# Kernel tuning notes

Measured on AMD Instinct MI355X. Metric: run time of the kernel, lower is better.

## Reference

```python
import jax, jax.numpy as jnp
import numpy as np

H = 768; R = 16; L = 3; NS = 128; NQ = 128


def setup_inputs():
    key = jax.random.key(0)
    ks = iter(jax.random.split(key, 40))
    def w(shape, s=0.02):
        return (s * jax.random.normal(next(ks), shape)).astype(jnp.float32)
    return {
        "support_features": jax.random.normal(next(ks), (NS, H), jnp.float32),
        "support_labels": jax.random.randint(next(ks), (NS,), 0, 3),
        "query_features": jax.random.normal(next(ks), (NQ, H), jnp.float32),
        "sim_w1": w((H, 2 * H)), "sim_b1": jnp.zeros((H,), jnp.float32),
        "sim_w2": w((R, H)), "sim_b2": jnp.zeros((R,), jnp.float32),
        "div_w1": w((H, 2 * H)), "div_b1": jnp.zeros((H,), jnp.float32),
        "div_w2": w((R, H)), "div_b2": jnp.zeros((R,), jnp.float32),
        "rel_w": w((L, R, H, H)), "rel_b": jnp.zeros((L, R, H), jnp.float32),
        "agg_w1": w((L, H, 2 * H)), "agg_b1": jnp.zeros((L, H), jnp.float32),
        "agg_w2": w((L, H, H)), "agg_b2": jnp.zeros((L, H), jnp.float32),
        "ln_g": jnp.ones((L, H), jnp.float32), "ln_b": jnp.zeros((L, H), jnp.float32),
        "cls_w1": w((H // 2, H)), "cls_b1": jnp.zeros((H // 2,), jnp.float32),
        "cls_w2": w((3, H // 2)), "cls_b2": jnp.zeros((3,), jnp.float32),
    }


def _symmetrize(F):
    # torch loop fills [i,j] and [j,i] with value computed from pair (min(i,j), max(i,j)); diag stays 0
    N = F.shape[0]
    idx = jnp.arange(N)
    lower = (idx[:, None] > idx[None, :])
    Fs = jnp.where(lower[:, :, None], jnp.swapaxes(F, 0, 1), F)
    off = (idx[:, None] != idx[None, :]).astype(F.dtype)
    return Fs * off[:, :, None]


def _relations(x, w1, b1, w2, b2, diversity):
    h = x.shape[1]
    wa, wb = w1[:, :h], w1[:, h:]  # split concat([a,b]) @ w1^T into two matmuls
    pa = x @ wa.T                  # [N,H], contribution of first element (x_i)
    if diversity:
        d = jnp.abs(x[:, None, :] - x[None, :, :])   # [N,N,H]
        hid = jax.nn.relu(pa[:, None, :] + d @ wb.T + b1)
    else:
        pb = x @ wb.T
        hid = jax.nn.relu(pa[:, None, :] + pb[None, :, :] + b1)
    logits = hid @ w2.T + b2       # [N,N,R]
    return _symmetrize(jax.nn.softmax(logits, axis=-1))


def _layer_norm(y, g, b):
    mu = y.mean(-1, keepdims=True)
    var = ((y - mu) ** 2).mean(-1, keepdims=True)
    return (y - mu) / jnp.sqrt(var + 1e-5) * g + b


def _prop_layer(x, C, rw, rb, aw1, ab1, aw2, ab2, g, b):
    N = x.shape[0]
    T = jnp.einsum('jh,rkh->jrk', x, rw) + rb       # per-relation transform [N,R,H]
    msg = jnp.einsum('ijr,jrk->ik', C, T) / (N - 1)  # mean over N-1 neighbors (diag of C is 0)
    comb = jnp.concatenate([x, msg], axis=-1)
    agg = jax.nn.relu(comb @ aw1.T + ab1) @ aw2.T + ab2
    return _layer_norm(agg + x, g, b)


def reference(support_features, support_labels, query_features,
              sim_w1, sim_b1, sim_w2, sim_b2,
              div_w1, div_b1, div_w2, div_b2,
              rel_w, rel_b, agg_w1, agg_b1, agg_w2, agg_b2, ln_g, ln_b,
              cls_w1, cls_b1, cls_w2, cls_b2):
    all_x = jnp.concatenate([support_features, query_features], axis=0)
    sim = _relations(all_x, sim_w1, sim_b1, sim_w2, sim_b2, diversity=False)
    div = _relations(all_x, div_w1, div_b1, div_w2, div_b2, diversity=True)
    C = (sim + div) * 0.5
    x = all_x
    for l in range(L):
        x = _prop_layer(x, C, rel_w[l], rel_b[l], agg_w1[l], agg_b1[l],
                        agg_w2[l], agg_b2[l], ln_g[l], ln_b[l])
    q = x[support_features.shape[0]:]
    preds = jax.nn.relu(q @ cls_w1.T + cls_b1) @ cls_w2.T + cls_b2  # dropout = identity (eval)
    return preds, sim, div, x
```

## Files before the change

kernel.cpp:

```cpp
#include <hip/hip_runtime.h>
#include <hip/hip_bf16.h>


typedef __attribute__((ext_vector_type(8))) short s16x8;
typedef __attribute__((ext_vector_type(4))) float f32x4;

__device__ __forceinline__ short f2bf_s(float f){
  union { __hip_bfloat16 h; short s; } u; u.h = __float2bfloat16(f); return u.s;
}
__device__ __forceinline__ float bf_s2f(short s){
  union { __hip_bfloat16 h; short s; } u; u.s = s; return __bfloat162float(u.h);
}
__device__ __forceinline__ f32x4 mfma16(s16x8 a, s16x8 b, f32x4 c){
  return __builtin_amdgcn_mfma_f32_16x16x32_bf16(a, b, c, 0, 0, 0);
}
__device__ __forceinline__ void gload16(void* lds, const void* g){
  __builtin_amdgcn_global_load_lds((const __attribute__((address_space(1))) void*)g,
                                   (__attribute__((address_space(3))) void*)lds,
                                   16, 0, 0);
}
__device__ __forceinline__ unsigned pack2bf(float lo, float hi){
  return __builtin_amdgcn_perm(__float_as_uint(hi), __float_as_uint(lo), 0x07060302u);
}
__device__ __forceinline__ s16x8 absdiff_bf(uint4 a, uint4 b){
  union { s16x8 v; unsigned u[4]; } o;
  const unsigned au[4] = {a.x,a.y,a.z,a.w}, bu[4] = {b.x,b.y,b.z,b.w};
  #pragma unroll
  for (int w = 0; w < 4; ++w){
    float dlo = __uint_as_float(au[w] << 16)         - __uint_as_float(bu[w] << 16);
    float dhi = __uint_as_float(au[w] & 0xffff0000u) - __uint_as_float(bu[w] & 0xffff0000u);
    unsigned r;
    asm("v_cvt_pk_bf16_f32 %0, abs(%1), abs(%2)" : "=v"(r) : "v"(dlo), "v"(dhi));
    o.u[w] = r;
  }
  return o.v;
}

__device__ __forceinline__ void tri_decode(int b, int& i0, int& j0){
  int jb = (int)((sqrtf(2.f*(float)b + 1.f) - 1.f)*0.5f);
  while (2*(jb+1)*(jb+2) <= b) ++jb;
  while (2*jb*(jb+1) > b) --jb;
  i0 = (b - 2*jb*(jb+1))*4;
  j0 = jb*16;
}

template<int BM, int BN, int EPI>
__global__ __launch_bounds__(256) void gemm_bt2(
    const short* __restrict__ A, int lda,
    const short* __restrict__ B, int ldb,
    float* __restrict__ Cf, short* __restrict__ Cb, int ldc,
    const float* __restrict__ bias, int K, int NT)
{
  __shared__ short As[BM*128];
  __shared__ short Bs[BN*128];
  const int tid = threadIdx.x, lane = tid & 63, wid = tid >> 6;
  const int nt = blockIdx.x % NT, mt = blockIdx.x / NT;
  const int m0 = mt*BM, n0 = nt*BN;
  const int wm0 = (wid>>1)*(BM/2), wn0 = (wid&1)*(BN/2);
  f32x4 acc[BM/32][BN/32] = {};
  for (int k0 = 0; k0 < K; k0 += 128){
    if (k0) __syncthreads();
    #pragma unroll
    for (int q = 0; q < BM/16; ++q){
      const int d = (wid*(BM/16)+q)*1024 + lane*16;
      const int row = d>>8, c = d&255;
      gload16((char*)As + (wid*(BM/16)+q)*1024,
              (const char*)A + (size_t)(m0+row)*lda*2 + (size_t)k0*2 + (c ^ ((row&7)<<4)));
    }
    #pragma unroll
    for (int q = 0; q < BN/16; ++q){
      const int d = (wid*(BN/16)+q)*1024 + lane*16;
      const int row = d>>8, c = d&255;
      gload16((char*)Bs + (wid*(BN/16)+q)*1024,
              (const char*)B + (size_t)(n0+row)*ldb*2 + (size_t)k0*2 + (c ^ ((row&7)<<4)));
    }
    __syncthreads();
    #pragma unroll
    for (int kk = 0; kk < 4; ++kk){
      const int colb = (kk*32 + (lane>>4)*8)*2;
      s16x8 af[BM/32], bfv[BN/32];
      #pragma unroll
      for (int mi = 0; mi < BM/32; ++mi){
        const int row = wm0 + mi*16 + (lane&15);
        af[mi] = *(const s16x8*)((char*)As + row*256 + (colb ^ ((row&7)<<4)));
      }
      #pragma unroll
      for (int ni = 0; ni < BN/32; ++ni){
        const int row = wn0 + ni*16 + (lane&15);
        bfv[ni] = *(const s16x8*)((char*)Bs + row*256 + (colb ^ ((row&7)<<4)));
      }
      #pragma unroll
      for (int mi = 0; mi < BM/32; ++mi)
        #pragma unroll
        for (int ni = 0; ni < BN/32; ++ni)
          acc[mi][ni] = mfma16(af[mi], bfv[ni], acc[mi][ni]);
    }
  }
  #pragma unroll
  for (int mi = 0; mi < BM/32; ++mi){
    #pragma unroll
    for (int ni = 0; ni < BN/32; ++ni){
      const int gcol = n0 + wn0 + ni*16 + (lane&15);
      const float bv = bias[gcol];
      #pragma unroll
      for (int r = 0; r < 4; ++r){
        const int grow = m0 + wm0 + mi*16 + (lane>>4)*4 + r;
        float v = acc[mi][ni][r] + bv;
        if (EPI == 2) v = fmaxf(v, 0.f);
        if (EPI == 3) Cf[(size_t)grow*ldc + gcol] = v;
        else          Cb[(size_t)grow*ldc + gcol] = f2bf_s(v);
      }
    }
  }
}

__global__ __launch_bounds__(256) void gemm_msg(
    const short* __restrict__ A,
    const short* __restrict__ B,
    float* __restrict__ slabs)
{
  __shared__ short As[64*64];
  __shared__ short Bs[64*64];
  const int tid = threadIdx.x, lane = tid & 63, wid = tid >> 6;
  const int mt = blockIdx.x / 12, nt = blockIdx.x % 12;
  const int m0 = mt*64, n0 = nt*64, kc0 = blockIdx.y*512;
  const int wm0 = (wid>>1)*32, wn0 = (wid&1)*32;
  f32x4 acc[2][2] = {};
  for (int s = 0; s < 8; ++s){
    const int k0 = kc0 + s*64;
    if (s) __syncthreads();
    #pragma unroll
    for (int q = 0; q < 2; ++q){
      const int d = (wid*2+q)*1024 + lane*16;
      const int row = d>>7, c = d&127;
      gload16((char*)As + (wid*2+q)*1024,
              (const char*)A + (size_t)(m0+row)*8192 + (size_t)k0*2 + (c ^ ((row&7)<<4)));
    }
    #pragma unroll
    for (int rd = 0; rd < 2; ++rd){
      int ei = rd*2048 + tid*8, kr = ei>>6, nc = ei&63;
      union { uint4 v; short s4[8]; } u;
      u.v = *(const uint4*)(B + (size_t)(k0+kr)*768 + n0 + nc);
      #pragma unroll
      for (int e = 0; e < 8; ++e)
        *(short*)((char*)Bs + (nc+e)*128 + ((kr*2) ^ (((nc+e)&7)<<4))) = u.s4[e];
    }
    __syncthreads();
    #pragma unroll
    for (int kk = 0; kk < 2; ++kk){
      const int colb = (kk*32 + (lane>>4)*8)*2;
      s16x8 af[2], bfv[2];
      #pragma unroll
      for (int mi = 0; mi < 2; ++mi){
        const int row = wm0 + mi*16 + (lane&15);
        af[mi] = *(const s16x8*)((char*)As + row*128 + (colb ^ ((row&7)<<4)));
      }
      #pragma unroll
      for (int ni = 0; ni < 2; ++ni){
        const int row = wn0 + ni*16 + (lane&15);
        bfv[ni] = *(const s16x8*)((char*)Bs + row*128 + (colb ^ ((row&7)<<4)));
      }
      #pragma unroll
      for (int mi = 0; mi < 2; ++mi)
        #pragma unroll
        for (int ni = 0; ni < 2; ++ni)
          acc[mi][ni] = mfma16(af[mi], bfv[ni], acc[mi][ni]);
    }
  }
  float* out = slabs + (size_t)blockIdx.y*196608;
  #pragma unroll
  for (int mi = 0; mi < 2; ++mi)
    #pragma unroll
    for (int ni = 0; ni < 2; ++ni){
      const int gcol = n0 + wn0 + ni*16 + (lane&15);
      #pragma unroll
      for (int r = 0; r < 4; ++r){
        const int grow = m0 + wm0 + mi*16 + (lane>>4)*4 + r;
        out[(size_t)grow*768 + gcol] = acc[mi][ni][r];
      }
    }
}

__global__ void msgsum(const float* __restrict__ slabs, short* __restrict__ comb){
  const int i = (blockIdx.x*256 + threadIdx.x)*4;
  if (i >= 196608) return;
  float4 s = {0.f,0.f,0.f,0.f};
  #pragma unroll
  for (int c = 0; c < 8; ++c){
    float4 v = *(const float4*)(slabs + (size_t)c*196608 + i);
    s.x += v.x; s.y += v.y; s.z += v.z; s.w += v.w;
  }
  const float sc = 1.f/255.f;
  const int row = i/768, col = i%768;
  union { uint2 u; short s4[4]; } o;
  o.s4[0]=f2bf_s(s.x*sc); o.s4[1]=f2bf_s(s.y*sc);
  o.s4[2]=f2bf_s(s.z*sc); o.s4[3]=f2bf_s(s.w*sc);
  *(uint2*)(comb + (size_t)row*1536 + 768 + col) = o.u;
}

__device__ __forceinline__ void stageB(short* dstbase, const short* Bsrc,
                                       int n0, int k0, int wv, int lane){
  #pragma unroll
  for (int q = 0; q < 8; ++q){
    const int d = (wv*8+q)*1024 + lane*16;
    const int row = d>>7, c = d&127;
    gload16((char*)dstbase + (wv*8+q)*1024,
            (const char*)Bsrc + (size_t)(n0+row)*1536 + (size_t)k0*2 + (c ^ ((row&7)<<4)));
  }
}

__global__ __launch_bounds__(256, 2) void pairrel3(
    const short* __restrict__ xb,
    const short* __restrict__ wbdiv,
    const float* __restrict__ P2,
    const short* __restrict__ w2d_g,
    float* __restrict__ Ldp)
{
  __shared__ short Bs[2*256*64];
  const int tid = threadIdx.x, lane = tid & 63, wv = tid >> 6;
  const int wm = wv >> 1, wc = wv & 1;
  int i0, j0; tri_decode(blockIdx.x, i0, j0);
  const int nt = blockIdx.y, n0 = nt*256;

  const short* xjp  = xb + (size_t)(j0 + (lane&15))*1536 + (lane>>4)*8;
  const short* xi0p = xb + (size_t)(i0 + wm*2    )*1536 + (lane>>4)*8;
  const short* xi1p = xb + (size_t)(i0 + wm*2 + 1)*1536 + (lane>>4)*8;

  stageB(Bs, wbdiv, n0, 0, wv, lane);

  f32x4 acc[2][8] = {};
  for (int t = 0; t < 12; ++t){
    if (t < 11) stageB(Bs + ((t+1)&1)*16384, wbdiv, n0, (t+1)*64, wv, lane);
    uint4 uja  = *(const uint4*)(xjp  + t*64);
    uint4 ujb  = *(const uint4*)(xjp  + t*64 + 32);
    uint4 ui0a = *(const uint4*)(xi0p + t*64);
    uint4 ui0b = *(const uint4*)(xi0p + t*64 + 32);
    uint4 ui1a = *(const uint4*)(xi1p + t*64);
    uint4 ui1b = *(const uint4*)(xi1p + t*64 + 32);
    __builtin_amdgcn_sched_barrier(0);
    if (t < 11) asm volatile("s_waitcnt vmcnt(8)" ::: "memory");
    else        asm volatile("s_waitcnt vmcnt(0)" ::: "memory");
    __builtin_amdgcn_s_barrier();
    __builtin_amdgcn_sched_barrier(0);
    const char* bufc = (const char*)Bs + (t&1)*32768;
    #pragma unroll
    for (int kk = 0; kk < 2; ++kk){
      s16x8 af0 = absdiff_bf(kk ? ujb : uja, kk ? ui0b : ui0a);
      s16x8 af1 = absdiff_bf(kk ? ujb : uja, kk ? ui1b : ui1a);
      const int colb = (kk*32 + (lane>>4)*8)*2;
      s16x8 bfv[8];
      #pragma unroll
      for (int ni = 0; ni < 8; ++ni){
        const int row = wc*128 + ni*16 + (lane&15);
        bfv[ni] = *(const s16x8*)(bufc + row*128 + (colb ^ ((row&7)<<4)));
      }
      #pragma unroll
      for (int ni = 0; ni < 8; ++ni){
        acc[0][ni] = mfma16(af0, bfv[ni], acc[0][ni]);
        acc[1][ni] = mfma16(af1, bfv[ni], acc[1][ni]);
      }
    }
    __builtin_amdgcn_sched_barrier(0);
    __builtin_amdgcn_s_barrier();
  }
  __syncthreads();
  #pragma unroll
  for (int mi = 0; mi < 2; ++mi){
    #pragma unroll
    for (int ni = 0; ni < 8; ++ni){
      const int col = wc*128 + ni*16 + (lane&15);
      const float pav = P2[(size_t)(i0 + wm*2 + mi)*2304 + 1536 + n0 + col];
      #pragma unroll
      for (int r = 0; r < 4; ++r){
        const int row = wm*32 + mi*16 + (lane>>4)*4 + r;
        const float v = fmaxf(acc[mi][ni][r] + pav, 0.f);
        *(short*)((char*)Bs + row*512 + ((col*2) ^ ((row&7)<<4))) =
            (short)(__float_as_uint(v) >> 16);
      }
    }
  }
  __syncthreads();
  f32x4 acc2 = {0.f,0.f,0.f,0.f};
  const int arow = wv*16 + (lane&15);
  #pragma unroll
  for (int q = 0; q < 8; ++q){
    const int colb = (q*32 + (lane>>4)*8)*2;
    s16x8 a = *(const s16x8*)((const char*)Bs + arow*512 + (colb ^ ((arow&7)<<4)));
    s16x8 w = *(const s16x8*)(w2d_g + (size_t)(lane&15)*768 + n0 + q*32 + (lane>>4)*8);
    acc2 = mfma16(a, w, acc2);
  }
  const int r_ = lane & 15;
  #pragma unroll
  for (int r = 0; r < 4; ++r){
    const int p = wv*16 + (lane>>4)*4 + r;
    const int i = i0 + (p>>4), j = j0 + (p&15);
    Ldp[(size_t)nt*1048576 + (((size_t)i<<8) + j)*16 + r_] = acc2[r];
  }
}

__global__ __launch_bounds__(256) void simpart(
    const float* __restrict__ P2,
    const short* __restrict__ w2s_g,
    float* __restrict__ Ls)
{
  __shared__ short Hs[64*256];
  const int tid = threadIdx.x, lane = tid & 63, wv = tid >> 6;
  int i0, j0; tri_decode(blockIdx.x, i0, j0);
  const int arow = wv*16 + (lane&15);
  f32x4 acc2 = {0.f,0.f,0.f,0.f};
  for (int nt = 0; nt < 3; ++nt){
    const int n0 = nt*256;
    if (nt) __syncthreads();
    {
      const int row = tid>>2, c0 = (tid&3)*64;
      const float* pap = P2 + (size_t)(i0 + (row>>4))*2304 + n0 + c0;
      const float* pbp = P2 + (size_t)(j0 + (row&15))*2304 + 768 + n0 + c0;
      #pragma unroll
      for (int cc = 0; cc < 64; cc += 8){
        float4 a0 = *(const float4*)(pap+cc), a1 = *(const float4*)(pap+cc+4);
        float4 q0 = *(const float4*)(pbp+cc), q1 = *(const float4*)(pbp+cc+4);
        uint4 o;
        o.x = pack2bf(fmaxf(a0.x+q0.x,0.f), fmaxf(a0.y+q0.y,0.f));
        o.y = pack2bf(fmaxf(a0.z+q0.z,0.f), fmaxf(a0.w+q0.w,0.f));
        o.z = pack2bf(fmaxf(a1.x+q1.x,0.f), fmaxf(a1.y+q1.y,0.f));
        o.w = pack2bf(fmaxf(a1.z+q1.z,0.f), fmaxf(a1.w+q1.w,0.f));
        *(uint4*)((char*)Hs + row*512 + (((c0+cc)*2) ^ ((row&7)<<4))) = o;
      }
    }
    __syncthreads();
    #pragma unroll
    for (int q = 0; q < 8; ++q){
      const int colb = (q*32 + (lane>>4)*8)*2;
      s16x8 a = *(const s16x8*)((const char*)Hs + arow*512 + (colb ^ ((arow&7)<<4)));
      s16x8 w = *(const s16x8*)(w2s_g + (size_t)(lane&15)*768 + n0 + q*32 + (lane>>4)*8);
      acc2 = mfma16(a, w, acc2);
    }
  }
  const int r_ = lane & 15;
  #pragma unroll
  for (int r = 0; r < 4; ++r){
    const int p = wv*16 + (lane>>4)*4 + r;
    const int i = i0 + (p>>4), j = j0 + (p&15);
    Ls[(((size_t)i<<8) + j)*16 + r_] = acc2[r];
  }
}

__global__ __launch_bounds__(256) void finisher2(
    const float* __restrict__ Ls, const float* __restrict__ Ldp,
    const float* __restrict__ b2s, const float* __restrict__ b2d,
    float* __restrict__ simo, float* __restrict__ divo, short* __restrict__ Cb)
{
  const int p = blockIdx.x*256 + threadIdx.x;
  const int i = p >> 8, j = p & 255;
  float so[16], dd[16];
  if (i == j){
    #pragma unroll
    for (int r = 0; r < 16; ++r){ so[r] = 0.f; dd[r] = 0.f; }
  } else {
    const int si = i < j ? i : j, sj = i < j ? j : i;
    const size_t base = (((size_t)si << 8) + sj) * 16;
    float mx = -1e30f, sum;
    #pragma unroll
    for (int r = 0; r < 16; ++r){ so[r] = Ls[base+r] + b2s[r]; mx = fmaxf(mx, so[r]); }
    sum = 0.f;
    #pragma unroll
    for (int r = 0; r < 16; ++r){ so[r] = expf(so[r]-mx); sum += so[r]; }
    sum = 1.f/sum;
    #pragma unroll
    for (int r = 0; r < 16; ++r) so[r] *= sum;
    mx = -1e30f;
    #pragma unroll
    for (int r = 0; r < 16; ++r){
      dd[r] = Ldp[base+r] + Ldp[base+r+1048576] + Ldp[base+r+2097152] + b2d[r];
      mx = fmaxf(mx, dd[r]);
    }
    sum = 0.f;
    #pragma unroll
    for (int r = 0; r < 16; ++r){ dd[r] = expf(dd[r]-mx); sum += dd[r]; }
    sum = 1.f/sum;
    #pragma unroll
    for (int r = 0; r < 16; ++r) dd[r] *= sum;
  }
  const size_t ob = (size_t)p * 16;
  #pragma unroll
  for (int r = 0; r < 16; ++r){
    simo[ob+r] = so[r];
    divo[ob+r] = dd[r];
    Cb[ob+r]   = f2bf_s(0.5f*(so[r]+dd[r]));
  }
}

__global__ __launch_bounds__(256) void gemm_relT(
    const short* __restrict__ A,
    const float* __restrict__ Bf,
    short* __restrict__ T,
    const float* __restrict__ bias)
{
  __shared__ short As[128*64];
  __shared__ short Bs[64*64];
  const int tid = threadIdx.x, lane = tid & 63, wv = tid >> 6;
  const int nt = blockIdx.x >> 1, mt = blockIdx.x & 1;
  const int n0 = nt*64, m0 = mt*128;
  const int wm = wv >> 1, wn = wv & 1;
  const int brow = tid >> 2, q4 = tid & 3;
  f32x4 acc[4][2] = {};
  for (int k0 = 0; k0 < 768; k0 += 64){
    if (k0) __syncthreads();
    #pragma unroll
    for (int q = 0; q < 4; ++q){
      const int d = (wv*4+q)*1024 + lane*16;
      const int row = d>>7, c = d&127;
      gload16((char*)As + (wv*4+q)*1024,
              (const char*)A + (size_t)(m0+row)*3072 + (size_t)k0*2 + (c ^ ((row&7)<<4)));
    }
    {
      const float* bp = Bf + (size_t)(n0+brow)*768 + k0 + q4*16;
      float4 v0 = *(const float4*)bp,      v1 = *(const float4*)(bp+4);
      float4 v2 = *(const float4*)(bp+8),  v3 = *(const float4*)(bp+12);
      union { uint4 v; unsigned u[4]; } ua, ub;
      ua.u[0]=pack2bf(v0.x,v0.y); ua.u[1]=pack2bf(v0.z,v0.w);
      ua.u[2]=pack2bf(v1.x,v1.y); ua.u[3]=pack2bf(v1.z,v1.w);
      ub.u[0]=pack2bf(v2.x,v2.y); ub.u[1]=pack2bf(v2.z,v2.w);
      ub.u[2]=pack2bf(v3.x,v3.y); ub.u[3]=pack2bf(v3.z,v3.w);
      const int bc = q4*32;
      *(uint4*)((char*)Bs + brow*128 + ((bc   ) ^ ((brow&7)<<4))) = ua.v;
      *(uint4*)((char*)Bs + brow*128 + ((bc+16) ^ ((brow&7)<<4))) = ub.v;
    }
    __syncthreads();
    #pragma unroll
    for (int kk = 0; kk < 2; ++kk){
      const int kb = kk*64 + (lane>>4)*16;
      s16x8 af[4], bfv[2];
      #pragma unroll
      for (int mi = 0; mi < 4; ++mi){
        const int row = wm*64 + mi*16 + (lane&15);
        af[mi] = *(const s16x8*)((char*)As + row*128 + (kb ^ ((row&7)<<4)));
      }
      #pragma unroll
      for (int ni = 0; ni < 2; ++ni){
        const int row = wn*32 + ni*16 + (lane&15);
        bfv[ni] = *(const s16x8*)((char*)Bs + row*128 + (kb ^ ((row&7)<<4)));
      }
      #pragma unroll
      for (int mi = 0; mi < 4; ++mi)
        #pragma unroll
        for (int ni = 0; ni < 2; ++ni)
          acc[mi][ni] = mfma16(af[mi], bfv[ni], acc[mi][ni]);
    }
  }
  #pragma unroll
  for (int mi = 0; mi < 4; ++mi)
    #pragma unroll
    for (int ni = 0; ni < 2; ++ni){
      const int nn = n0 + wn*32 + ni*16 + (lane&15);
      const float bv = bias[nn];
      #pragma unroll
      for (int r = 0; r < 4; ++r){
        const int row = m0 + wm*64 + mi*16 + (lane>>4)*4 + r;
        T[(size_t)row*12288 + nn] = f2bf_s(acc[mi][ni][r] + bv);
      }
    }
}

__global__ __launch_bounds__(256) void ln_kernel(
    const float* __restrict__ y, float* __restrict__ x, short* __restrict__ combx,
    const float* __restrict__ g, const float* __restrict__ b, float* __restrict__ xfinal)
{
  const int row = blockIdx.x, tid = threadIdx.x;
  float tv[3]; float s = 0.f, s2 = 0.f;
  #pragma unroll
  for (int c = 0; c < 3; ++c){
    const int idx = tid + c*256;
    const float v = y[row*768+idx] + x[row*768+idx];
    tv[c] = v; s += v; s2 += v*v;
  }
  #pragma unroll
  for (int off = 32; off > 0; off >>= 1){ s += __shfl_down(s, off); s2 += __shfl_down(s2, off); }
  __shared__ float red[8];
  const int wid = tid >> 6, lane = tid & 63;
  if (lane == 0){ red[wid] = s; red[wid+4] = s2; }
  __syncthreads();
  if (tid == 0){
    red[0] = red[0]+red[1]+red[2]+red[3];
    red[4] = red[4]+red[5]+red[6]+red[7];
  }
  __syncthreads();
  const float mu = red[0]*(1.f/768.f);
  const float var = red[4]*(1.f/768.f) - mu*mu;
  const float inv = rsqrtf(var + 1e-5f);
  #pragma unroll
  for (int c = 0; c < 3; ++c){
    const int idx = tid + c*256;
    const float v = (tv[c]-mu)*inv*g[idx] + b[idx];
    x[row*768+idx] = v;
    combx[(size_t)row*1536 + idx] = f2bf_s(v);
    if (xfinal) xfinal[row*768+idx] = v;
  }
}

__device__ __forceinline__ void cvt4(const float* __restrict__ s,
                                     short* __restrict__ d, int i, int n){
  if (i >= n) return;
  float4 v = *(const float4*)(s+i);
  union { uint2 u; short s4[4]; } o;
  o.s4[0]=f2bf_s(v.x); o.s4[1]=f2bf_s(v.y); o.s4[2]=f2bf_s(v.z); o.s4[3]=f2bf_s(v.w);
  *(uint2*)(d+i) = o.u;
}

__global__ void setup_all(
    const float* __restrict__ sim_w2, const float* __restrict__ div_w2,
    const float* __restrict__ agg_w1, const float* __restrict__ agg_w2,
    const float* __restrict__ cls_w1, const float* __restrict__ sim_w1,
    const float* __restrict__ div_w1, const float* __restrict__ sup,
    const float* __restrict__ qry, const float* __restrict__ sim_b1,
    const float* __restrict__ div_b1,
    short* __restrict__ W2S, short* __restrict__ W2D, short* __restrict__ AW1,
    short* __restrict__ AW2, short* __restrict__ CW1, short* __restrict__ W1X4,
    float* __restrict__ XF, short* __restrict__ COMB, float* __restrict__ B1C)
{
  const int b = blockIdx.x, tid = threadIdx.x;
  if (b < 12)        cvt4(sim_w2, W2S, (b*256+tid)*4, 12288);
  else if (b < 24)   cvt4(div_w2, W2D, ((b-12)*256+tid)*4, 12288);
  else if (b < 3480) cvt4(agg_w1, AW1, ((b-24)*256+tid)*4, 3538944);
  else if (b < 5208) cvt4(agg_w2, AW2, ((b-3480)*256+tid)*4, 1769472);
  else if (b < 5496) cvt4(cls_w1, CW1, ((b-5208)*256+tid)*4, 294912);
  else if (b < 7800){
    const int i = ((b-5496)*256+tid)*4;
    if (i < 2359296){
      const int mat = i / 589824, rem = i % 589824;
      const int r = rem / 768, c = rem % 768;
      const float* src = (mat < 2 ? sim_w1 : div_w1) + (size_t)r*1536 + (mat&1)*768 + c;
      float4 v = *(const float4*)src;
      union { uint2 u; short s4[4]; } o;
      o.s4[0]=f2bf_s(v.x); o.s4[1]=f2bf_s(v.y); o.s4[2]=f2bf_s(v.z); o.s4[3]=f2bf_s(v.w);
      *(uint2*)(W1X4+i) = o.u;
    }
  } else if (b < 7992){
    const int i = ((b-7800)*256+tid)*4;
    if (i < 196608){
      const int row = i / 768, col = i % 768;
      const float* s = (row < 128 ? sup + (size_t)row*768 : qry + (size_t)(row-128)*768) + col;
      float4 v = *(const float4*)s;
      *(float4*)(XF+i) = v;
      union { uint2 u; short s4[4]; } o;
      o.s4[0]=f2bf_s(v.x); o.s4[1]=f2bf_s(v.y); o.s4[2]=f2bf_s(v.z); o.s4[3]=f2bf_s(v.w);
      *(uint2*)(COMB + (size_t)row*1536 + col) = o.u;
    }
  } else {
    for (int t = tid; t < 2304; t += 256)
      B1C[t] = (t < 768) ? sim_b1[t] : ((t < 1536) ? 0.f : div_b1[t-1536]);
  }
}

__global__ void cls2_kernel(const short* __restrict__ hc, const float* __restrict__ w2,
                            const float* __restrict__ b2, float* __restrict__ preds){
  const int t = blockIdx.x*192 + threadIdx.x;
  if (t >= 384) return;
  const int m = t/3, c = t - m*3;
  float s = b2[c];
  for (int k = 0; k < 384; ++k)
    s += bf_s2f(hc[m*384+k]) * w2[c*384+k];
  preds[m*3+c] = s;
}

static const size_t OFF_B1CAT = 0;
static const size_t OFF_LS    = 16384;
static const size_t OFF_MSGF  = 4210688;
static const size_t OFF_LDP   = 10502144;
static const size_t OFF_P     = 23085056;
static const size_t OFF_XF    = 25444352;
static const size_t OFF_Y     = 26230784;
static const size_t OFF_COMB  = 27017216;
static const size_t OFF_CB    = 27803648;
static const size_t OFF_W1X4  = 29900800;
static const size_t OFF_W2S   = 34619392;
static const size_t OFF_W2D   = 34643968;
static const size_t OFF_AW1   = 34668544;
static const size_t OFF_AW2   = 41746432;
static const size_t OFF_CW1   = 45285376;
static const size_t OFF_TBUF  = 45875200;
static const size_t OFF_HID1  = 52166656;
static const size_t OFF_HIDC  = 52559872;

extern "C" void kernel_launch(void* const* d_in, const int* in_sizes, int n_in,
                              void* d_out, int out_size, void* d_ws, size_t ws_size,
                              hipStream_t stream)
{
  (void)in_sizes; (void)n_in; (void)out_size; (void)ws_size;
  const float* sup    = (const float*)d_in[0];
  const float* qry    = (const float*)d_in[2];
  const float* sim_w1 = (const float*)d_in[3];
  const float* sim_b1 = (const float*)d_in[4];
  const float* sim_w2 = (const float*)d_in[5];
  const float* sim_b2 = (const float*)d_in[6];
  const float* div_w1 = (const float*)d_in[7];
  const float* div_b1 = (const float*)d_in[8];
  const float* div_w2 = (const float*)d_in[9];
  const float* div_b2 = (const float*)d_in[10];
  const float* rel_w  = (const float*)d_in[11];
  const float* rel_b  = (const float*)d_in[12];
  const float* agg_w1 = (const float*)d_in[13];
  const float* agg_b1 = (const float*)d_in[14];
  const float* agg_w2 = (const float*)d_in[15];
  const float* agg_b2 = (const float*)d_in[16];
  const float* ln_g   = (const float*)d_in[17];
  const float* ln_b   = (const float*)d_in[18];
  const float* cls_w1 = (const float*)d_in[19];
  const float* cls_b1 = (const float*)d_in[20];
  const float* cls_w2 = (const float*)d_in[21];
  const float* cls_b2 = (const float*)d_in[22];

  char* w = (char*)d_ws;
  float* B1C  = (float*)(w + OFF_B1CAT);
  float* LS   = (float*)(w + OFF_LS);
  float* MSGF = (float*)(w + OFF_MSGF);
  float* LDP  = (float*)(w + OFF_LDP);
  float* P2   = (float*)(w + OFF_P);
  float* XF   = (float*)(w + OFF_XF);
  float* Y    = (float*)(w + OFF_Y);
  short* COMB = (short*)(w + OFF_COMB);
  short* CB   = (short*)(w + OFF_CB);
  short* W1X4 = (short*)(w + OFF_W1X4);
  short* W2S  = (short*)(w + OFF_W2S);
  short* W2D  = (short*)(w + OFF_W2D);
  short* AW1  = (short*)(w + OFF_AW1);
  short* AW2  = (short*)(w + OFF_AW2);
  short* CW1  = (short*)(w + OFF_CW1);
  short* TBUF = (short*)(w + OFF_TBUF);
  short* HID1 = (short*)(w + OFF_HID1);
  short* HIDC = (short*)(w + OFF_HIDC);

  float* preds = (float*)d_out;
  float* simo  = preds + 384;
  float* divo  = simo + 1048576;
  float* xout  = divo + 1048576;

  setup_all<<<7993, 256, 0, stream>>>(sim_w2, div_w2, agg_w1, agg_w2, cls_w1,
                                      sim_w1, div_w1, sup, qry, sim_b1, div_b1,
                                      W2S, W2D, AW1, AW2, CW1, W1X4, XF, COMB, B1C);

  gemm_bt2<64,64,3><<<144, 256, 0, stream>>>(COMB, 1536, W1X4, 768, P2, nullptr, 2304,
                                             B1C, 768, 36);

  pairrel3<<<dim3(544,3), 256, 0, stream>>>(COMB, W1X4 + (size_t)3*589824, P2, W2D, LDP);
  simpart<<<544, 256, 0, stream>>>(P2, W2S, LS);
  finisher2<<<256, 256, 0, stream>>>(LS, LDP, sim_b2, div_b2, simo, divo, CB);

  for (int l = 0; l < 3; ++l){
    gemm_relT<<<384, 256, 0, stream>>>(COMB, rel_w + (size_t)l*9437184, TBUF,
                                       rel_b + l*12288);
    gemm_msg<<<dim3(48,8), 256, 0, stream>>>(CB, TBUF, MSGF);
    msgsum<<<192, 256, 0, stream>>>(MSGF, COMB);
    gemm_bt2<32,32,2><<<192, 256, 0, stream>>>(COMB, 1536, AW1 + (size_t)l*1179648, 1536,
                                               nullptr, HID1, 768, agg_b1 + l*768, 1536, 24);
    gemm_bt2<32,32,3><<<192, 256, 0, stream>>>(HID1, 768, AW2 + (size_t)l*589824, 768,
                                               Y, nullptr, 768, agg_b2 + l*768, 768, 24);
    ln_kernel<<<256, 256, 0, stream>>>(Y, XF, COMB, ln_g + l*768, ln_b + l*768,
                                       (l == 2) ? xout : nullptr);
  }

  gemm_bt2<32,32,2><<<48, 256, 0, stream>>>(COMB + (size_t)128*1536, 1536, CW1, 768,
                                            nullptr, HIDC, 384, cls_b1, 768, 12);
  cls2_kernel<<<2, 192, 0, stream>>>(HIDC, cls_w2, cls_b2, preds);
}
```

Measured before the change: 320.7 us.

## Double pair-relation tile to 4x32 with 512-thread blocks sharing staged weights

The diversity pair-relation kernel now handles 4x32 (i,j) pair tiles per block with 8 waves, in place of 4x16 tiles with 4 waves. Each staged tile of the div weight slab is therefore reused by twice as many pairs, which halves the global weight traffic per pair and the block count. The second-stage R-projection is done in two halves, with a split-K LDS reduction between wave groups. The costs are more barriers in the epilogue, a heavier per-block register and occupancy demand from launch bounds (512,4), and a new triangular decode.

```diff
diff --git a/kernel.cpp b/kernel.cpp
--- a/kernel.cpp
+++ b/kernel.cpp
@@ -42,6 +42,13 @@
   while (2*jb*(jb+1) > b) --jb;
   i0 = (b - 2*jb*(jb+1))*4;
   j0 = jb*16;
+}
+__device__ __forceinline__ void tri_decode32(int b, int& i0, int& j0){
+  int jb = (int)((sqrtf((float)b + 1.f) - 1.f)*0.5f);
+  while (4*(jb+1)*(jb+2) <= b) ++jb;
+  while (4*jb*(jb+1) > b) --jb;
+  i0 = (b - 4*jb*(jb+1))*4;
+  j0 = jb*32;
 }
 
 template<int BM, int BN, int EPI>
@@ -198,18 +205,7 @@
   *(uint2*)(comb + (size_t)row*1536 + 768 + col) = o.u;
 }
 
-__device__ __forceinline__ void stageB(short* dstbase, const short* Bsrc,
-                                       int n0, int k0, int wv, int lane){
-  #pragma unroll
-  for (int q = 0; q < 8; ++q){
-    const int d = (wv*8+q)*1024 + lane*16;
-    const int row = d>>7, c = d&127;
-    gload16((char*)dstbase + (wv*8+q)*1024,
-            (const char*)Bsrc + (size_t)(n0+row)*1536 + (size_t)k0*2 + (c ^ ((row&7)<<4)));
-  }
-}
-
-__global__ __launch_bounds__(256, 2) void pairrel3(
+__global__ __launch_bounds__(512, 4) void pairrel4(
     const short* __restrict__ xb,
     const short* __restrict__ wbdiv,
     const float* __restrict__ P2,
@@ -218,28 +214,43 @@
 {
   __shared__ short Bs[2*256*64];
   const int tid = threadIdx.x, lane = tid & 63, wv = tid >> 6;
-  const int wm = wv >> 1, wc = wv & 1;
-  int i0, j0; tri_decode(blockIdx.x, i0, j0);
+  const int ip = wv >> 2, jj = (wv >> 1) & 1, wc = wv & 1;
+  int i0, j0; tri_decode32(blockIdx.x, i0, j0);
   const int nt = blockIdx.y, n0 = nt*256;
 
-  const short* xjp  = xb + (size_t)(j0 + (lane&15))*1536 + (lane>>4)*8;
-  const short* xi0p = xb + (size_t)(i0 + wm*2    )*1536 + (lane>>4)*8;
-  const short* xi1p = xb + (size_t)(i0 + wm*2 + 1)*1536 + (lane>>4)*8;
-
-  stageB(Bs, wbdiv, n0, 0, wv, lane);
+  const short* xjp  = xb + (size_t)(j0 + jj*16 + (lane&15))*1536 + (lane>>4)*8;
+  const short* xi0p = xb + (size_t)(i0 + 2*ip    )*1536 + (lane>>4)*8;
+  const short* xi1p = xb + (size_t)(i0 + 2*ip + 1)*1536 + (lane>>4)*8;
+
+  #pragma unroll
+  for (int q = 0; q < 4; ++q){
+    const int d = (wv*4+q)*1024 + lane*16;
+    const int row = d>>7, c = d&127;
+    gload16((char*)Bs + (wv*4+q)*1024,
+            (const char*)wbdiv + (size_t)(n0+row)*1536 + (c ^ ((row&7)<<4)));
+  }
 
   f32x4 acc[2][8] = {};
   for (int t = 0; t < 12; ++t){
-    if (t < 11) stageB(Bs + ((t+1)&1)*16384, wbdiv, n0, (t+1)*64, wv, lane);
     uint4 uja  = *(const uint4*)(xjp  + t*64);
     uint4 ujb  = *(const uint4*)(xjp  + t*64 + 32);
     uint4 ui0a = *(const uint4*)(xi0p + t*64);
     uint4 ui0b = *(const uint4*)(xi0p + t*64 + 32);
     uint4 ui1a = *(const uint4*)(xi1p + t*64);
     uint4 ui1b = *(const uint4*)(xi1p + t*64 + 32);
+    if (t < 11){
+      char* dst = (char*)Bs + ((t+1)&1)*32768;
+      const char* src = (const char*)wbdiv + (size_t)(t+1)*128;
+      #pragma unroll
+      for (int q = 0; q < 4; ++q){
+        const int d = (wv*4+q)*1024 + lane*16;
+        const int row = d>>7, c = d&127;
+        gload16(dst + (wv*4+q)*1024, src + (size_t)(n0+row)*1536 + (c ^ ((row&7)<<4)));
+      }
+    }
     __builtin_amdgcn_sched_barrier(0);
-    if (t < 11) asm volatile("s_waitcnt vmcnt(8)" ::: "memory");
-    else        asm volatile("s_waitcnt vmcnt(0)" ::: "memory");
+    if (t < 11) asm volatile("s_waitcnt vmcnt(10)" ::: "memory");
+    else        asm volatile("s_waitcnt vmcnt(6)"  ::: "memory");
     __builtin_amdgcn_s_barrier();
     __builtin_amdgcn_sched_barrier(0);
     const char* bufc = (const char*)Bs + (t&1)*32768;
@@ -248,53 +259,68 @@
       s16x8 af0 = absdiff_bf(kk ? ujb : uja, kk ? ui0b : ui0a);
       s16x8 af1 = absdiff_bf(kk ? ujb : uja, kk ? ui1b : ui1a);
       const int colb = (kk*32 + (lane>>4)*8)*2;
-      s16x8 bfv[8];
       #pragma unroll
       for (int ni = 0; ni < 8; ++ni){
         const int row = wc*128 + ni*16 + (lane&15);
-        bfv[ni] = *(const s16x8*)(bufc + row*128 + (colb ^ ((row&7)<<4)));
-      }
-      #pragma unroll
-      for (int ni = 0; ni < 8; ++ni){
-        acc[0][ni] = mfma16(af0, bfv[ni], acc[0][ni]);
-        acc[1][ni] = mfma16(af1, bfv[ni], acc[1][ni]);
+        s16x8 bv = *(const s16x8*)(bufc + row*128 + (colb ^ ((row&7)<<4)));
+        acc[0][ni] = mfma16(af0, bv, acc[0][ni]);
+        acc[1][ni] = mfma16(af1, bv, acc[1][ni]);
       }
     }
     __builtin_amdgcn_sched_barrier(0);
     __builtin_amdgcn_s_barrier();
   }
   __syncthreads();
-  #pragma unroll
-  for (int mi = 0; mi < 2; ++mi){
-    #pragma unroll
-    for (int ni = 0; ni < 8; ++ni){
-      const int col = wc*128 + ni*16 + (lane&15);
-      const float pav = P2[(size_t)(i0 + wm*2 + mi)*2304 + 1536 + n0 + col];
+
+  float* red = (float*)((char*)Bs + 32768);
+  #pragma unroll
+  for (int h = 0; h < 2; ++h){
+    if (ip == h){
+      #pragma unroll
+      for (int mi = 0; mi < 2; ++mi){
+        const float* pr = P2 + (size_t)(i0 + 2*h + mi)*2304 + 1536 + n0;
+        #pragma unroll
+        for (int ni = 0; ni < 8; ++ni){
+          const int col = wc*128 + ni*16 + (lane&15);
+          const float pav = pr[col];
+          #pragma unroll
+          for (int r = 0; r < 4; ++r){
+            const int lrow = mi*32 + jj*16 + (lane>>4)*4 + r;
+            const float v = fmaxf(acc[mi][ni][r] + pav, 0.f);
+            *(short*)((char*)Bs + lrow*512 + ((col*2) ^ ((lrow&7)<<4))) =
+                (short)(__float_as_uint(v) >> 16);
+          }
+        }
+      }
+    }
+    __syncthreads();
+    const int kh = wv >> 2, rq = wv & 3;
+    f32x4 a2 = {0.f,0.f,0.f,0.f};
+    const int arow = rq*16 + (lane&15);
+    #pragma unroll
+    for (int q = 0; q < 4; ++q){
+      const int k = kh*128 + q*32 + (lane>>4)*8;
+      s16x8 a = *(const s16x8*)((char*)Bs + arow*512 + ((k*2) ^ ((arow&7)<<4)));
+      s16x8 w = *(const s16x8*)(w2d_g + (size_t)(lane&15)*768 + n0 + k);
+      a2 = mfma16(a, w, a2);
+    }
+    if (kh == 1){
+      #pragma unroll
+      for (int r = 0; r < 4; ++r)
+        red[(rq*16 + (lane>>4)*4 + r)*16 + (lane&15)] = a2[r];
+    }
+    __syncthreads();
+    if (kh == 0){
       #pragma unroll
       for (int r = 0; r < 4; ++r){
-        const int row = wm*32 + mi*16 + (lane>>4)*4 + r;
-        const float v = fmaxf(acc[mi][ni][r] + pav, 0.f);
-        *(short*)((char*)Bs + row*512 + ((col*2) ^ ((row&7)<<4))) =
-            (short)(__float_as_uint(v) >> 16);
-      }
-    }
-  }
-  __syncthreads();
-  f32x4 acc2 = {0.f,0.f,0.f,0.f};
-  const int arow = wv*16 + (lane&15);
-  #pragma unroll
-  for (int q = 0; q < 8; ++q){
-    const int colb = (q*32 + (lane>>4)*8)*2;
-    s16x8 a = *(const s16x8*)((const char*)Bs + arow*512 + (colb ^ ((arow&7)<<4)));
-    s16x8 w = *(const s16x8*)(w2d_g + (size_t)(lane&15)*768 + n0 + q*32 + (lane>>4)*8);
-    acc2 = mfma16(a, w, acc2);
-  }
-  const int r_ = lane & 15;
-  #pragma unroll
-  for (int r = 0; r < 4; ++r){
-    const int p = wv*16 + (lane>>4)*4 + r;
-    const int i = i0 + (p>>4), j = j0 + (p&15);
-    Ldp[(size_t)nt*1048576 + (((size_t)i<<8) + j)*16 + r_] = acc2[r];
+        const int lrow = rq*16 + (lane>>4)*4 + r;
+        const int p = h*64 + lrow;
+        const int i = i0 + (p>>5), j = j0 + (p&31);
+        Ldp[(size_t)nt*1048576 + (((size_t)i<<8) + j)*16 + (lane&15)]
+          = a2[r] + red[lrow*16 + (lane&15)];
+      }
+    }
+    __syncthreads();
   }
 }
 
@@ -642,7 +668,7 @@
   gemm_bt2<64,64,3><<<144, 256, 0, stream>>>(COMB, 1536, W1X4, 768, P2, nullptr, 2304,
                                              B1C, 768, 36);
 
-  pairrel3<<<dim3(544,3), 256, 0, stream>>>(COMB, W1X4 + (size_t)3*589824, P2, W2D, LDP);
+  pairrel4<<<dim3(288,3), 512, 0, stream>>>(COMB, W1X4 + (size_t)3*589824, P2, W2D, LDP);
   simpart<<<544, 256, 0, stream>>>(P2, W2S, LS);
   finisher2<<<256, 256, 0, stream>>>(LS, LDP, sim_b2, div_b2, simo, divo, CB);
 
```

Result: faster. 305.3 us (median of 2 runs) (-4.8%).
